# Optimization experiments

Hardware: AMD Instinct MI355X
Metric: run time of the kernel (lower is better)

Reference implementation:

```python
import jax, jax.numpy as jnp
import numpy as np

N = 50000
E = 800000
G = 64
H, C = 16, 4  # heads, out_channels per head; H*C = 64


def setup_inputs() -> dict:
    key = jax.random.key(0)
    ks = jax.random.split(key, 16)
    return {
        "x": jax.random.normal(ks[0], (N,), jnp.float32),
        "edge_index": jax.random.randint(ks[1], (2, E), 0, N),
        "edge_attr": jax.random.normal(ks[2], (E,), jnp.float32),
        "batch": jnp.sort(jax.random.randint(ks[3], (N,), 0, G)),
        # GATv2Conv(1 -> 4, heads=16, edge_dim=1, concat=True)
        "Wl": jax.random.normal(ks[4], (1, H * C), jnp.float32) * 0.5,
        "bl": jnp.full((H * C,), 0.01, jnp.float32),
        "Wr": jax.random.normal(ks[5], (1, H * C), jnp.float32) * 0.5,
        "br": jnp.full((H * C,), 0.01, jnp.float32),
        "We": jax.random.normal(ks[6], (1, H * C), jnp.float32) * 0.5,
        "att": jax.random.normal(ks[7], (H, C), jnp.float32) * 0.5,
        "gat_bias": jnp.zeros((H * C,), jnp.float32),
        # GraphNorm(64)
        "gn_w": jnp.ones((H * C,), jnp.float32),
        "gn_b": jnp.zeros((H * C,), jnp.float32),
        "gn_ms": jnp.ones((H * C,), jnp.float32),
        # SAGEConv(64 -> 64, mean aggr, root weight)
        "sage_Wl": jax.random.normal(ks[8], (H * C, 64), jnp.float32) * 0.125,
        "sage_bl": jnp.full((64,), 0.01, jnp.float32),
        "sage_Wr": jax.random.normal(ks[9], (H * C, 64), jnp.float32) * 0.125,
        # MLP head
        "fc1_W": jax.random.normal(ks[10], (128, 2048), jnp.float32) * 0.08,
        "fc1_b": jnp.full((2048,), 0.01, jnp.float32),
        "fc2_W": jax.random.normal(ks[11], (2048, 1024), jnp.float32) * 0.02,
        "fc2_b": jnp.full((1024,), 0.01, jnp.float32),
        "fc3_W": jax.random.normal(ks[12], (1024, 3), jnp.float32) * 0.03,
        "fc3_b": jnp.full((3,), 0.01, jnp.float32),
    }


def reference(x, edge_index, edge_attr, batch, Wl, bl, Wr, br, We, att, gat_bias,
              gn_w, gn_b, gn_ms, sage_Wl, sage_bl, sage_Wr,
              fc1_W, fc1_b, fc2_W, fc2_b, fc3_W, fc3_b):
    src0, dst0 = edge_index[0], edge_index[1]
    x1 = x[:, None]  # [N,1] (torch.unsqueeze(x, -1))
    # ---- GATv2Conv ----
    xl = (x1 @ Wl + bl).reshape(N, H, C)  # source-side (x_j, also the value)
    xr = (x1 @ Wr + br).reshape(N, H, C)  # target-side (x_i)
    # add self loops; fill_value='mean' -> per-node mean of incoming edge_attr
    deg_in = jax.ops.segment_sum(jnp.ones((E,), x.dtype), dst0, num_segments=N)
    loop_attr = jax.ops.segment_sum(edge_attr, dst0, num_segments=N) / jnp.maximum(deg_in, 1.0)
    loops = jnp.arange(N)
    src = jnp.concatenate([src0, loops])
    dst = jnp.concatenate([dst0, loops])
    ea = jnp.concatenate([edge_attr, loop_attr])[:, None]  # [E+N,1]
    e = (ea @ We).reshape(-1, H, C)
    m = jax.nn.leaky_relu(xl[src] + xr[dst] + e, 0.2)  # [E+N,H,C]
    score = jnp.einsum('ehc,hc->eh', m, att)
    smax = jax.ops.segment_max(score, dst, num_segments=N)
    a = jnp.exp(score - smax[dst])
    denom = jax.ops.segment_sum(a, dst, num_segments=N)
    alpha = a / denom[dst]  # segmented softmax over incoming edges
    h = jax.ops.segment_sum(alpha[:, :, None] * xl[src], dst, num_segments=N)
    h = h.reshape(N, H * C) + gat_bias
    h = jax.nn.relu(h)
    # ---- GraphNorm ----
    cnt = jax.ops.segment_sum(jnp.ones((N,), x.dtype), batch, num_segments=G)[:, None]
    mean = jax.ops.segment_sum(h, batch, num_segments=G) / cnt
    o = h - mean[batch] * gn_ms
    var = jax.ops.segment_sum(o * o, batch, num_segments=G) / cnt
    h = gn_w * o / jnp.sqrt(var[batch] + 1e-5) + gn_b
    # ---- SAGEConv (mean aggregation + root weight) ----
    neigh = jax.ops.segment_sum(h[src0], dst0, num_segments=N) / jnp.maximum(deg_in, 1.0)[:, None]
    h = neigh @ sage_Wl + sage_bl + h @ sage_Wr
    h = jax.nn.relu(h)
    # ---- global max + mean pooling, MLP head (eval mode: dropout off) ----
    gmax = jax.ops.segment_max(h, batch, num_segments=G)
    gmean = jax.ops.segment_sum(h, batch, num_segments=G) / cnt
    g = jnp.concatenate([gmax, gmean], axis=1)  # [G, 128]
    g = jax.nn.relu(g @ fc1_W + fc1_b)
    g = jax.nn.relu(g @ fc2_W + fc2_b)
    return g @ fc3_W + fc3_b
```

## Files before the change

kernel.cpp:

```cpp
#include <hip/hip_runtime.h>

#define GG 64
#define HH 16
#define KK 64
#define S_SUB 8

__device__ __forceinline__ float bf2f(unsigned short u){
  return __uint_as_float(((unsigned)u) << 16);
}
__device__ __forceinline__ unsigned short f2bf(float f){
  unsigned u = __float_as_uint(f);
  unsigned r = u + 0x7fffu + ((u >> 16) & 1u);
  return (unsigned short)(r >> 16);
}


__global__ void k_count_rank(const int* __restrict__ ei, int* deg, int* __restrict__ rank, int E){
  int e = blockIdx.x*blockDim.x + threadIdx.x;
  if (e < E) rank[e] = atomicAdd(&deg[ei[E + e]], 1);
}

__global__ void k_scan1(const int* __restrict__ deg, int* __restrict__ bsum, int N){
  int base = blockIdx.x*1024;
  int lim = min(base + 1024, N);
  int s = 0;
  for (int i = base + (int)threadIdx.x; i < lim; i += 256) s += deg[i];
  #pragma unroll
  for (int ofs = 32; ofs >= 1; ofs >>= 1) s += __shfl_down(s, ofs, 64);
  __shared__ int ws[4];
  int lane = threadIdx.x & 63, wv = threadIdx.x >> 6;
  if (lane == 0) ws[wv] = s;
  __syncthreads();
  if (threadIdx.x == 0) bsum[blockIdx.x] = ws[0] + ws[1] + ws[2] + ws[3];
}

__global__ void __launch_bounds__(1024)
k_scan2(int* __restrict__ bsum, int* __restrict__ row_start_N, int NB){
  int t = threadIdx.x;
  int v = (t < NB) ? bsum[t] : 0;
  int lane = t & 63, wv = t >> 6;
  int val = v;
  #pragma unroll
  for (int ofs = 1; ofs < 64; ofs <<= 1){
    int tt = __shfl_up(val, ofs, 64);
    if (lane >= ofs) val += tt;
  }
  __shared__ int ws[16];
  if (lane == 63) ws[wv] = val;
  __syncthreads();
  if (t == 0){
    int run = 0;
    #pragma unroll
    for (int w = 0; w < 16; ++w){ int tmp = ws[w]; ws[w] = run; run += tmp; }
  }
  __syncthreads();
  int excl = ws[wv] + val - v;
  if (t < NB) bsum[t] = excl;
  if (t == NB - 1) *row_start_N = excl + v;
}

__global__ void k_scan3(const int* __restrict__ deg, const int* __restrict__ bsum,
                        int* __restrict__ row_start, int N){
  int b = blockIdx.x;
  int base = b*1024 + (int)threadIdx.x*4;
  int d0 = (base+0 < N) ? deg[base+0] : 0;
  int d1 = (base+1 < N) ? deg[base+1] : 0;
  int d2 = (base+2 < N) ? deg[base+2] : 0;
  int d3 = (base+3 < N) ? deg[base+3] : 0;
  int s = d0 + d1 + d2 + d3;
  int lane = threadIdx.x & 63, wv = threadIdx.x >> 6;
  int val = s;
  #pragma unroll
  for (int ofs = 1; ofs < 64; ofs <<= 1){
    int tt = __shfl_up(val, ofs, 64);
    if (lane >= ofs) val += tt;
  }
  __shared__ int ws[4];
  if (lane == 63) ws[wv] = val;
  __syncthreads();
  if (threadIdx.x == 0){
    int run = 0;
    #pragma unroll
    for (int w = 0; w < 4; ++w){ int tmp = ws[w]; ws[w] = run; run += tmp; }
  }
  __syncthreads();
  int pre = bsum[b] + ws[wv] + val - s;
  if (base+0 < N){ row_start[base+0] = pre; pre += d0; }
  if (base+1 < N){ row_start[base+1] = pre; pre += d1; }
  if (base+2 < N){ row_start[base+2] = pre; pre += d2; }
  if (base+3 < N){ row_start[base+3] = pre; }
}

__global__ void k_scatter(const int* __restrict__ ei, const float* __restrict__ ea,
                          const int* __restrict__ row_start, const int* __restrict__ rank,
                          int2* __restrict__ csr_se, int E){
  int e = blockIdx.x*blockDim.x + threadIdx.x;
  if (e >= E) return;
  int d = ei[E + e];
  int pos = row_start[d] + rank[e];
  csr_se[pos] = make_int2(ei[e], __float_as_int(ea[e]));
}

__global__ void k_gbounds(const int* __restrict__ batch, int N, int* __restrict__ goff){
  int g = threadIdx.x;
  if (g > GG) return;
  int lo = 0, hi = N;
  while (lo < hi){ int mid = (lo+hi) >> 1; if (batch[mid] < g) lo = mid+1; else hi = mid; }
  goff[g] = lo;
}

__global__ void k_gat(const float* __restrict__ x, const int* __restrict__ row_start,
                      const int2* __restrict__ cse,
                      const float* __restrict__ Wl, const float* __restrict__ bl,
                      const float* __restrict__ Wr, const float* __restrict__ br,
                      const float* __restrict__ We, const float* __restrict__ att,
                      const float* __restrict__ gat_bias,
                      float* __restrict__ h, int N){
  int t = blockIdx.x*blockDim.x + threadIdx.x;
  int n   = t >> 2;
  int sub = t & 3;
  if (n >= N) return;
  float xd = x[n];
  float wl[16], we[16], at[16], pre[16];
  int k0 = sub*16;
  #pragma unroll
  for (int i = 0; i < 16; ++i){
    int k = k0 + i;
    wl[i] = Wl[k]; we[i] = We[k]; at[i] = att[k];
    pre[i] = bl[k] + fmaf(xd, Wr[k], br[k]);
  }
  int e0 = row_start[n], e1 = row_start[n+1];
  float m[4]  = {-3.4e38f,-3.4e38f,-3.4e38f,-3.4e38f};
  float den[4] = {0,0,0,0}, S1[4] = {0,0,0,0};
  float asum = 0.f;

#define PROC(XS, EAV)                                                        \
  { float xs_ = (XS), ea_ = (EAV);                                           \
    _Pragma("unroll")                                                        \
    for (int hi2 = 0; hi2 < 4; ++hi2){                                       \
      float sc = 0.f;                                                        \
      _Pragma("unroll")                                                      \
      for (int c = 0; c < 4; ++c){                                           \
        int i = hi2*4 + c;                                                   \
        float tt = fmaf(xs_, wl[i], fmaf(ea_, we[i], pre[i]));               \
        tt = (tt > 0.f) ? tt : 0.2f*tt;                                      \
        sc = fmaf(tt, at[i], sc);                                            \
      }                                                                      \
      float nm = fmaxf(m[hi2], sc);                                          \
      float corr = __expf(m[hi2] - nm);                                      \
      float a    = __expf(sc - nm);                                          \
      den[hi2] = den[hi2]*corr + a;                                          \
      S1[hi2]  = S1[hi2] *corr + a*xs_;                                      \
      m[hi2] = nm; } }

  int e = e0;
  for (; e + 1 < e1; e += 2){
    int2 p0 = cse[e], p1 = cse[e+1];
    float xs0 = x[p0.x], xs1 = x[p1.x];
    float ea0 = __int_as_float(p0.y), ea1 = __int_as_float(p1.y);
    asum += ea0 + ea1;
    PROC(xs0, ea0);
    PROC(xs1, ea1);
  }
  if (e < e1){
    int2 p0 = cse[e];
    float xs0 = x[p0.x], ea0 = __int_as_float(p0.y);
    asum += ea0;
    PROC(xs0, ea0);
  }
  {
    float degf = (float)(e1 - e0);
    float eav = asum / fmaxf(degf, 1.0f);
    PROC(xd, eav);
  }
#undef PROC
  #pragma unroll
  for (int hi2 = 0; hi2 < 4; ++hi2){
    float r = S1[hi2] / den[hi2];
    float4 o;
    #pragma unroll
    for (int c = 0; c < 4; ++c){
      int i = hi2*4 + c, k = k0 + i;
      float v = fmaxf(fmaf(wl[i], r, bl[k] + gat_bias[k]), 0.f);
      ((float*)&o)[c] = v;
    }
    *(float4*)(h + (size_t)n*KK + k0 + hi2*4) = o;
  }
}

__global__ void k_gstats_part(const float* __restrict__ h, const int* __restrict__ goff,
                              float* __restrict__ gsum, float* __restrict__ gsum2){
  int g = blockIdx.x, sb = blockIdx.y;
  int s = goff[g], epos = goff[g+1];
  int k = threadIdx.x & 63, slice = threadIdx.x >> 6;
  float sum = 0.f, sum2 = 0.f;
  for (int n = s + sb*4 + slice; n < epos; n += S_SUB*4){
    float v = h[(size_t)n*KK + k];
    sum += v; sum2 += v*v;
  }
  __shared__ float ls[4][KK], ls2[4][KK];
  ls[slice][k] = sum; ls2[slice][k] = sum2;
  __syncthreads();
  if (slice == 0){
    float a  = ls[0][k]+ls[1][k]+ls[2][k]+ls[3][k];
    float b2 = ls2[0][k]+ls2[1][k]+ls2[2][k]+ls2[3][k];
    atomicAdd(&gsum[g*KK + k], a);
    atomicAdd(&gsum2[g*KK + k], b2);
  }
}

__global__ void k_gncoef(const float* __restrict__ gsum, const float* __restrict__ gsum2,
                         const int* __restrict__ goff,
                         const float* __restrict__ gn_w, const float* __restrict__ gn_b,
                         const float* __restrict__ gn_ms,
                         float* __restrict__ scale, float* __restrict__ shift){
  int i = blockIdx.x*blockDim.x + threadIdx.x;
  if (i >= GG*KK) return;
  int g = i >> 6, k = i & 63;
  float c = fmaxf((float)(goff[g+1] - goff[g]), 1.0f);
  float mean = gsum[i]/c;
  float eh2  = gsum2[i]/c;
  float ms = gn_ms[k];
  float var = eh2 - 2.f*ms*mean*mean + ms*ms*mean*mean;
  float sc = gn_w[k] / sqrtf(var + 1e-5f);
  scale[i] = sc;
  shift[i] = gn_b[k] - sc*mean*ms;
}

__global__ void k_norm(float* __restrict__ h, unsigned short* __restrict__ hb,
                       const int* __restrict__ batch,
                       const float* __restrict__ scale, const float* __restrict__ shift, int N){
  int gid = blockIdx.x*blockDim.x + threadIdx.x;
  if (gid >= N*KK) return;
  int n = gid >> 6, k = gid & 63;
  int b = batch[n];
  float v = fmaf(scale[b*KK + k], h[gid], shift[b*KK + k]);
  h[gid] = v;
  hb[gid] = f2bf(v);
}

__global__ void k_sage(const float* __restrict__ h, const unsigned short* __restrict__ hb,
                       const int* __restrict__ row_start, const int2* __restrict__ cse,
                       const float* __restrict__ Wl, const float* __restrict__ bln,
                       const float* __restrict__ Wr,
                       float* __restrict__ h2, int N){
  __shared__ float snm[16][KK], shn[16][KK];
  const ushort4* hb4 = (const ushort4*)hb;
  int tid = threadIdx.x;
  int u = tid >> 4;
  int q = tid & 15;
  int n = blockIdx.x*16 + u;
  if (n < N){
    int e0 = row_start[n], e1 = row_start[n+1];
    float a0=0.f,a1=0.f,a2=0.f,a3=0.f;
    float b0=0.f,b1=0.f,b2=0.f,b3=0.f;
    int e = e0;
    for (; e + 3 < e1; e += 4){
      int s0 = cse[e].x, s1 = cse[e+1].x, s2 = cse[e+2].x, s3 = cse[e+3].x;
      ushort4 v0 = hb4[(size_t)s0*16 + q];
      ushort4 v1 = hb4[(size_t)s1*16 + q];
      ushort4 v2 = hb4[(size_t)s2*16 + q];
      ushort4 v3 = hb4[(size_t)s3*16 + q];
      a0 += bf2f(v0.x); a1 += bf2f(v0.y); a2 += bf2f(v0.z); a3 += bf2f(v0.w);
      b0 += bf2f(v1.x); b1 += bf2f(v1.y); b2 += bf2f(v1.z); b3 += bf2f(v1.w);
      a0 += bf2f(v2.x); a1 += bf2f(v2.y); a2 += bf2f(v2.z); a3 += bf2f(v2.w);
      b0 += bf2f(v3.x); b1 += bf2f(v3.y); b2 += bf2f(v3.z); b3 += bf2f(v3.w);
    }
    for (; e < e1; ++e){
      ushort4 v0 = hb4[(size_t)cse[e].x*16 + q];
      a0 += bf2f(v0.x); a1 += bf2f(v0.y); a2 += bf2f(v0.z); a3 += bf2f(v0.w);
    }
    float dg = fmaxf((float)(e1 - e0), 1.0f);
    float inv = 1.0f/dg;
    float4 nm = make_float4((a0+b0)*inv, (a1+b1)*inv, (a2+b2)*inv, (a3+b3)*inv);
    *(float4*)&snm[u][q*4] = nm;
    *(float4*)&shn[u][q*4] = *(const float4*)(h + (size_t)n*KK + q*4);
  }
  __syncthreads();
  int j = tid & 63, u0 = tid >> 6;
  float acc[4];
  #pragma unroll
  for (int p = 0; p < 4; ++p) acc[p] = bln[j];
  for (int k = 0; k < KK; ++k){
    float wlv = Wl[k*KK + j], wrv = Wr[k*KK + j];
    #pragma unroll
    for (int p = 0; p < 4; ++p){
      int un = u0 + p*4;
      acc[p] = fmaf(snm[un][k], wlv, acc[p]);
      acc[p] = fmaf(shn[un][k], wrv, acc[p]);
    }
  }
  #pragma unroll
  for (int p = 0; p < 4; ++p){
    int un = u0 + p*4;
    int nn = blockIdx.x*16 + un;
    if (nn < N) h2[(size_t)nn*KK + j] = fmaxf(acc[p], 0.f);
  }
}

__global__ void k_pool_part(const float* __restrict__ h2, const int* __restrict__ goff,
                            unsigned* __restrict__ gmaxu, float* __restrict__ gsumP){
  int g = blockIdx.x, sb = blockIdx.y;
  int s = goff[g], epos = goff[g+1];
  int k = threadIdx.x & 63, slice = threadIdx.x >> 6;
  float mx = 0.f, sm = 0.f;
  for (int n = s + sb*4 + slice; n < epos; n += S_SUB*4){
    float v = h2[(size_t)n*KK + k];
    mx = fmaxf(mx, v); sm += v;
  }
  __shared__ float lm[4][KK], lsum[4][KK];
  lm[slice][k] = mx; lsum[slice][k] = sm;
  __syncthreads();
  if (slice == 0){
    float m2 = fmaxf(fmaxf(lm[0][k], lm[1][k]), fmaxf(lm[2][k], lm[3][k]));
    float s2 = lsum[0][k]+lsum[1][k]+lsum[2][k]+lsum[3][k];
    atomicMax(&gmaxu[g*KK + k], __float_as_uint(m2));
    atomicAdd(&gsumP[g*KK + k], s2);
  }
}

__global__ void k_poolfin(const unsigned* __restrict__ gmaxu, const float* __restrict__ gsumP,
                          const int* __restrict__ goff, float* __restrict__ gvec){
  int i = blockIdx.x*blockDim.x + threadIdx.x;
  if (i >= GG*128) return;
  int g = i >> 7, j = i & 127;
  float c = fmaxf((float)(goff[g+1] - goff[g]), 1.0f);
  gvec[i] = (j < 64) ? __uint_as_float(gmaxu[g*64 + j])
                     : gsumP[g*64 + (j-64)] / c;
}


__global__ void k_fc1(const float* __restrict__ in, const float* __restrict__ W,
                      const float* __restrict__ b, float* __restrict__ out){
  __shared__ float sin[128];
  int g = blockIdx.y, jt = blockIdx.x;
  int tid = threadIdx.x;
  if (tid < 128) sin[tid] = in[g*128 + tid];
  __syncthreads();
  int j = jt*256 + tid;
  float acc = b[j];
  #pragma unroll 16
  for (int k = 0; k < 128; ++k)
    acc = fmaf(sin[k], W[(size_t)k*2048 + j], acc);
  out[(size_t)g*2048 + j] = fmaxf(acc, 0.f);
}

__global__ void k_fc2a(const float* __restrict__ in, const float* __restrict__ W,
                       float* __restrict__ partial){
  __shared__ float sin[64][128];
  int jt = blockIdx.x, ks = blockIdx.y;
  int k0 = ks*128;
  int tid = threadIdx.x;
  for (int idx = tid; idx < 64*128; idx += 256){
    int g = idx >> 7, k = idx & 127;
    sin[g][k] = in[(size_t)g*2048 + k0 + k];
  }
  __syncthreads();
  int j = tid & 63, gs = tid >> 6;
  const float* Wp = W + (size_t)k0*1024 + jt*64 + j;
  float acc[16];
  #pragma unroll
  for (int p = 0; p < 16; ++p) acc[p] = 0.f;
  for (int k = 0; k < 128; ++k){
    float w = Wp[(size_t)k*1024];
    #pragma unroll
    for (int p = 0; p < 16; ++p)
      acc[p] = fmaf(sin[gs*16 + p][k], w, acc[p]);
  }
  #pragma unroll
  for (int p = 0; p < 16; ++p){
    int g = gs*16 + p;
    partial[((size_t)ks*64 + g)*1024 + jt*64 + j] = acc[p];
  }
}

__global__ void k_fc2red(const float* __restrict__ partial, const float* __restrict__ b,
                         float* __restrict__ out){
  int i = blockIdx.x*blockDim.x + threadIdx.x;
  int g = i >> 10, j = i & 1023;
  float s = b[j];
  #pragma unroll
  for (int ks = 0; ks < 16; ++ks)
    s += partial[((size_t)ks*64 + g)*1024 + j];
  out[i] = fmaxf(s, 0.f);
}

__global__ void k_fc3(const float* __restrict__ in, const float* __restrict__ W,
                      const float* __restrict__ b, float* __restrict__ out, int nOut){
  int w = (blockIdx.x*blockDim.x + threadIdx.x) >> 6;
  int lane = threadIdx.x & 63;
  if (w >= GG*nOut) return;
  int g = w / nOut, j = w - g*nOut;
  const float* row = in + (size_t)g*1024;
  float acc = 0.f;
  #pragma unroll
  for (int k = lane; k < 1024; k += 64)
    acc = fmaf(row[k], W[(size_t)k*nOut + j], acc);
  #pragma unroll
  for (int ofs = 32; ofs >= 1; ofs >>= 1)
    acc += __shfl_down(acc, ofs, 64);
  if (lane == 0) out[w] = acc + b[j];
}

extern "C" void kernel_launch(void* const* d_in, const int* in_sizes, int n_in,
                              void* d_out, int out_size, void* d_ws, size_t ws_size,
                              hipStream_t stream) {
  const float* x        = (const float*)d_in[0];
  const int*   ei       = (const int*)d_in[1];
  const float* ea       = (const float*)d_in[2];
  const int*   batch    = (const int*)d_in[3];
  const float* Wl       = (const float*)d_in[4];
  const float* bl       = (const float*)d_in[5];
  const float* Wr       = (const float*)d_in[6];
  const float* br       = (const float*)d_in[7];
  const float* We       = (const float*)d_in[8];
  const float* att      = (const float*)d_in[9];
  const float* gat_bias = (const float*)d_in[10];
  const float* gn_w     = (const float*)d_in[11];
  const float* gn_b     = (const float*)d_in[12];
  const float* gn_ms    = (const float*)d_in[13];
  const float* sage_Wl  = (const float*)d_in[14];
  const float* sage_bl  = (const float*)d_in[15];
  const float* sage_Wr  = (const float*)d_in[16];
  const float* fc1_W    = (const float*)d_in[17];
  const float* fc1_b    = (const float*)d_in[18];
  const float* fc2_W    = (const float*)d_in[19];
  const float* fc2_b    = (const float*)d_in[20];
  const float* fc3_W    = (const float*)d_in[21];
  const float* fc3_b    = (const float*)d_in[22];

  const int N = in_sizes[0];
  const int E = in_sizes[1] / 2;
  const int NB = (N + 1023) / 1024;

  char* ws = (char*)d_ws;
  size_t off = 0;
  auto alloc = [&](size_t bytes){ void* p = ws + off; off += (bytes + 255) & ~(size_t)255; return p; };

  int*      deg_i  = (int*)alloc((size_t)N*4);
  float*    gsum   = (float*)alloc(GG*KK*4);
  float*    gsum2  = (float*)alloc(GG*KK*4);
  unsigned* gmaxu  = (unsigned*)alloc(GG*KK*4);
  float*    gsumP  = (float*)alloc(GG*KK*4);
  size_t zero_bytes = off;
  int*   rank      = (int*)alloc((size_t)E*4);
  int*   bsum      = (int*)alloc((size_t)NB*4);
  int*   row_start = (int*)alloc((size_t)(N+1)*4);
  int*   goff      = (int*)alloc((GG+1)*4);
  int2*  csr_se    = (int2*)alloc((size_t)E*8);
  float* h         = (float*)alloc((size_t)N*KK*4);
  unsigned short* hb = (unsigned short*)alloc((size_t)N*KK*2);
  float* h2        = (float*)alloc((size_t)N*KK*4);
  float* scale     = (float*)alloc(GG*KK*4);
  float* shift     = (float*)alloc(GG*KK*4);
  float* gvec      = (float*)alloc(GG*128*4);
  float* out1      = (float*)alloc((size_t)GG*2048*4);
  float* out2      = (float*)alloc((size_t)GG*1024*4);
  float* partial   = (float*)alloc((size_t)16*GG*1024*4);
  (void)ws_size; (void)n_in; (void)out_size;

  hipMemsetAsync(d_ws, 0, zero_bytes, stream);

  const int B = 256;
  k_count_rank<<<(E+B-1)/B, B, 0, stream>>>(ei, deg_i, rank, E);
  k_gbounds<<<1, 128, 0, stream>>>(batch, N, goff);
  k_scan1  <<<NB, B, 0, stream>>>(deg_i, bsum, N);
  k_scan2  <<<1, 1024, 0, stream>>>(bsum, row_start + N, NB);
  k_scan3  <<<NB, B, 0, stream>>>(deg_i, bsum, row_start, N);
  k_scatter<<<(E+B-1)/B, B, 0, stream>>>(ei, ea, row_start, rank, csr_se, E);
  k_gat    <<<((size_t)N*4+B-1)/B, B, 0, stream>>>(x, row_start, csr_se,
                                                   Wl, bl, Wr, br, We, att, gat_bias, h, N);
  {
    dim3 grid(GG, S_SUB);
    k_gstats_part<<<grid, 256, 0, stream>>>(h, goff, gsum, gsum2);
  }
  k_gncoef <<<(GG*KK+B-1)/B, B, 0, stream>>>(gsum, gsum2, goff, gn_w, gn_b, gn_ms, scale, shift);
  k_norm   <<<((size_t)N*KK+B-1)/B, B, 0, stream>>>(h, hb, batch, scale, shift, N);
  k_sage   <<<(N+15)/16, B, 0, stream>>>(h, hb, row_start, csr_se, sage_Wl, sage_bl, sage_Wr, h2, N);
  {
    dim3 grid(GG, S_SUB);
    k_pool_part<<<grid, 256, 0, stream>>>(h2, goff, gmaxu, gsumP);
  }
  k_poolfin<<<(GG*128+B-1)/B, B, 0, stream>>>(gmaxu, gsumP, goff, gvec);
  {
    dim3 grid(8, GG);
    k_fc1  <<<grid, 256, 0, stream>>>(gvec, fc1_W, fc1_b, out1);
  }
  {
    dim3 grid(16, 16);
    k_fc2a <<<grid, 256, 0, stream>>>(out1, fc2_W, partial);
  }
  k_fc2red <<<(GG*1024+B-1)/B, B, 0, stream>>>(partial, fc2_b, out2);
  k_fc3    <<<(GG*3*64+B-1)/B, B, 0, stream>>>(out2, fc3_W, fc3_b, (float*)d_out, 3);
}
```

Baseline: 212.6 us.

## Fuse GraphNorm coefficients into norm kernel, fold pool finalize into fc1, deepen unrolls

Removes the k_gncoef and k_poolfin launches. The GraphNorm scale and shift are now computed inside a float4-vectorized k_norm, and the pooled vector is assembled inside k_fc1. The GAT edge loop is unrolled to 4 and the SAGE gather loop to 8 to expose more memory-level parallelism. This trades recomputing the coefficients in every thread and higher register pressure for two fewer kernel launches and fewer intermediate buffers.

```diff
diff --git a/kernel.cpp b/kernel.cpp
--- a/kernel.cpp
+++ b/kernel.cpp
@@ -154,15 +154,18 @@
       m[hi2] = nm; } }
 
   int e = e0;
-  for (; e + 1 < e1; e += 2){
-    int2 p0 = cse[e], p1 = cse[e+1];
-    float xs0 = x[p0.x], xs1 = x[p1.x];
+  for (; e + 3 < e1; e += 4){
+    int2 p0 = cse[e], p1 = cse[e+1], p2 = cse[e+2], p3 = cse[e+3];
+    float xs0 = x[p0.x], xs1 = x[p1.x], xs2 = x[p2.x], xs3 = x[p3.x];
     float ea0 = __int_as_float(p0.y), ea1 = __int_as_float(p1.y);
-    asum += ea0 + ea1;
+    float ea2 = __int_as_float(p2.y), ea3 = __int_as_float(p3.y);
+    asum += (ea0 + ea1) + (ea2 + ea3);
     PROC(xs0, ea0);
     PROC(xs1, ea1);
-  }
-  if (e < e1){
+    PROC(xs2, ea2);
+    PROC(xs3, ea3);
+  }
+  for (; e < e1; ++e){
     int2 p0 = cse[e];
     float xs0 = x[p0.x], ea0 = __int_as_float(p0.y);
     asum += ea0;
@@ -209,34 +212,35 @@
   }
 }
 
-__global__ void k_gncoef(const float* __restrict__ gsum, const float* __restrict__ gsum2,
-                         const int* __restrict__ goff,
-                         const float* __restrict__ gn_w, const float* __restrict__ gn_b,
-                         const float* __restrict__ gn_ms,
-                         float* __restrict__ scale, float* __restrict__ shift){
-  int i = blockIdx.x*blockDim.x + threadIdx.x;
-  if (i >= GG*KK) return;
-  int g = i >> 6, k = i & 63;
-  float c = fmaxf((float)(goff[g+1] - goff[g]), 1.0f);
-  float mean = gsum[i]/c;
-  float eh2  = gsum2[i]/c;
-  float ms = gn_ms[k];
-  float var = eh2 - 2.f*ms*mean*mean + ms*ms*mean*mean;
-  float sc = gn_w[k] / sqrtf(var + 1e-5f);
-  scale[i] = sc;
-  shift[i] = gn_b[k] - sc*mean*ms;
-}
-
 __global__ void k_norm(float* __restrict__ h, unsigned short* __restrict__ hb,
                        const int* __restrict__ batch,
-                       const float* __restrict__ scale, const float* __restrict__ shift, int N){
-  int gid = blockIdx.x*blockDim.x + threadIdx.x;
-  if (gid >= N*KK) return;
-  int n = gid >> 6, k = gid & 63;
+                       const float* __restrict__ gsum, const float* __restrict__ gsum2,
+                       const int* __restrict__ goff,
+                       const float* __restrict__ gn_w, const float* __restrict__ gn_b,
+                       const float* __restrict__ gn_ms, int N){
+  int t = blockIdx.x*blockDim.x + threadIdx.x;
+  if (t >= N*16) return;
+  int n = t >> 4, q = t & 15;
   int b = batch[n];
-  float v = fmaf(scale[b*KK + k], h[gid], shift[b*KK + k]);
-  h[gid] = v;
-  hb[gid] = f2bf(v);
+  float c = fmaxf((float)(goff[b+1] - goff[b]), 1.0f);
+  float inv = 1.0f / c;
+  float4 hv = *(float4*)(h + (size_t)n*KK + q*4);
+  float ov[4];
+  #pragma unroll
+  for (int i = 0; i < 4; ++i){
+    int k = q*4 + i;
+    float mean = gsum[b*KK + k]*inv;
+    float eh2  = gsum2[b*KK + k]*inv;
+    float ms = gn_ms[k];
+    float var = eh2 - 2.f*ms*mean*mean + ms*ms*mean*mean;
+    float sc = gn_w[k] * __frsqrt_rn(var + 1e-5f);
+    float sh = gn_b[k] - sc*mean*ms;
+    ov[i] = fmaf(sc, ((float*)&hv)[i], sh);
+  }
+  *(float4*)(h + (size_t)n*KK + q*4) = make_float4(ov[0], ov[1], ov[2], ov[3]);
+  ushort4 bv;
+  bv.x = f2bf(ov[0]); bv.y = f2bf(ov[1]); bv.z = f2bf(ov[2]); bv.w = f2bf(ov[3]);
+  *(ushort4*)(hb + (size_t)n*KK + q*4) = bv;
 }
 
 __global__ void k_sage(const float* __restrict__ h, const unsigned short* __restrict__ hb,
@@ -255,16 +259,25 @@
     float a0=0.f,a1=0.f,a2=0.f,a3=0.f;
     float b0=0.f,b1=0.f,b2=0.f,b3=0.f;
     int e = e0;
-    for (; e + 3 < e1; e += 4){
-      int s0 = cse[e].x, s1 = cse[e+1].x, s2 = cse[e+2].x, s3 = cse[e+3].x;
+    for (; e + 7 < e1; e += 8){
+      int s0 = cse[e].x,   s1 = cse[e+1].x, s2 = cse[e+2].x, s3 = cse[e+3].x;
+      int s4 = cse[e+4].x, s5 = cse[e+5].x, s6 = cse[e+6].x, s7 = cse[e+7].x;
       ushort4 v0 = hb4[(size_t)s0*16 + q];
       ushort4 v1 = hb4[(size_t)s1*16 + q];
       ushort4 v2 = hb4[(size_t)s2*16 + q];
       ushort4 v3 = hb4[(size_t)s3*16 + q];
+      ushort4 v4 = hb4[(size_t)s4*16 + q];
+      ushort4 v5 = hb4[(size_t)s5*16 + q];
+      ushort4 v6 = hb4[(size_t)s6*16 + q];
+      ushort4 v7 = hb4[(size_t)s7*16 + q];
       a0 += bf2f(v0.x); a1 += bf2f(v0.y); a2 += bf2f(v0.z); a3 += bf2f(v0.w);
       b0 += bf2f(v1.x); b1 += bf2f(v1.y); b2 += bf2f(v1.z); b3 += bf2f(v1.w);
       a0 += bf2f(v2.x); a1 += bf2f(v2.y); a2 += bf2f(v2.z); a3 += bf2f(v2.w);
       b0 += bf2f(v3.x); b1 += bf2f(v3.y); b2 += bf2f(v3.z); b3 += bf2f(v3.w);
+      a0 += bf2f(v4.x); a1 += bf2f(v4.y); a2 += bf2f(v4.z); a3 += bf2f(v4.w);
+      b0 += bf2f(v5.x); b1 += bf2f(v5.y); b2 += bf2f(v5.z); b3 += bf2f(v5.w);
+      a0 += bf2f(v6.x); a1 += bf2f(v6.y); a2 += bf2f(v6.z); a3 += bf2f(v6.w);
+      b0 += bf2f(v7.x); b1 += bf2f(v7.y); b2 += bf2f(v7.z); b3 += bf2f(v7.w);
     }
     for (; e < e1; ++e){
       ushort4 v0 = hb4[(size_t)cse[e].x*16 + q];
@@ -319,23 +332,19 @@
   }
 }
 
-__global__ void k_poolfin(const unsigned* __restrict__ gmaxu, const float* __restrict__ gsumP,
-                          const int* __restrict__ goff, float* __restrict__ gvec){
-  int i = blockIdx.x*blockDim.x + threadIdx.x;
-  if (i >= GG*128) return;
-  int g = i >> 7, j = i & 127;
-  float c = fmaxf((float)(goff[g+1] - goff[g]), 1.0f);
-  gvec[i] = (j < 64) ? __uint_as_float(gmaxu[g*64 + j])
-                     : gsumP[g*64 + (j-64)] / c;
-}
-
-
-__global__ void k_fc1(const float* __restrict__ in, const float* __restrict__ W,
-                      const float* __restrict__ b, float* __restrict__ out){
+
+__global__ void k_fc1(const unsigned* __restrict__ gmaxu, const float* __restrict__ gsumP,
+                      const int* __restrict__ goff,
+                      const float* __restrict__ W, const float* __restrict__ b,
+                      float* __restrict__ out){
   __shared__ float sin[128];
   int g = blockIdx.y, jt = blockIdx.x;
   int tid = threadIdx.x;
-  if (tid < 128) sin[tid] = in[g*128 + tid];
+  if (tid < 128){
+    float c = fmaxf((float)(goff[g+1] - goff[g]), 1.0f);
+    sin[tid] = (tid < 64) ? __uint_as_float(gmaxu[g*64 + tid])
+                          : gsumP[g*64 + (tid-64)] / c;
+  }
   __syncthreads();
   int j = jt*256 + tid;
   float acc = b[j];
@@ -451,9 +460,6 @@
   float* h         = (float*)alloc((size_t)N*KK*4);
   unsigned short* hb = (unsigned short*)alloc((size_t)N*KK*2);
   float* h2        = (float*)alloc((size_t)N*KK*4);
-  float* scale     = (float*)alloc(GG*KK*4);
-  float* shift     = (float*)alloc(GG*KK*4);
-  float* gvec      = (float*)alloc(GG*128*4);
   float* out1      = (float*)alloc((size_t)GG*2048*4);
   float* out2      = (float*)alloc((size_t)GG*1024*4);
   float* partial   = (float*)alloc((size_t)16*GG*1024*4);
@@ -474,17 +480,16 @@
     dim3 grid(GG, S_SUB);
     k_gstats_part<<<grid, 256, 0, stream>>>(h, goff, gsum, gsum2);
   }
-  k_gncoef <<<(GG*KK+B-1)/B, B, 0, stream>>>(gsum, gsum2, goff, gn_w, gn_b, gn_ms, scale, shift);
-  k_norm   <<<((size_t)N*KK+B-1)/B, B, 0, stream>>>(h, hb, batch, scale, shift, N);
+  k_norm   <<<((size_t)N*16+B-1)/B, B, 0, stream>>>(h, hb, batch, gsum, gsum2, goff,
+                                                    gn_w, gn_b, gn_ms, N);
   k_sage   <<<(N+15)/16, B, 0, stream>>>(h, hb, row_start, csr_se, sage_Wl, sage_bl, sage_Wr, h2, N);
   {
     dim3 grid(GG, S_SUB);
     k_pool_part<<<grid, 256, 0, stream>>>(h2, goff, gmaxu, gsumP);
   }
-  k_poolfin<<<(GG*128+B-1)/B, B, 0, stream>>>(gmaxu, gsumP, goff, gvec);
   {
     dim3 grid(8, GG);
-    k_fc1  <<<grid, 256, 0, stream>>>(gvec, fc1_W, fc1_b, out1);
+    k_fc1  <<<grid, 256, 0, stream>>>(gmaxu, gsumP, goff, fc1_W, fc1_b, out1);
   }
   {
     dim3 grid(16, 16);
```

Result: faster. 207.3 us (-2.5%).
